# Optimization experiments

Measured on AMD Instinct MI355X. Metric: run time of the kernel, lower is better.

## Reference

```python
import jax, jax.numpy as jnp
import numpy as np

S, T, B, IN, H, O = 64, 32, 512, 66, 1024, 1024  # S == max_length


def _gru_cell(x, h, Wih, Whh, bih, bhh):
    # PyTorch GRU cell: gates ordered (r, z, n)
    gi = x @ Wih.T + bih            # [B, 3H]
    gh = h @ Whh.T + bhh            # [B, 3H]
    ir, iz, inn = jnp.split(gi, 3, axis=1)
    hr, hz, hn = jnp.split(gh, 3, axis=1)
    r = jax.nn.sigmoid(ir + hr)
    z = jax.nn.sigmoid(iz + hz)
    n = jnp.tanh(inn + r * hn)
    return (1.0 - z) * n + z * h


def setup_inputs() -> dict:
    key = jax.random.key(0)
    ks = jax.random.split(key, 20)
    s = 0.02
    return {
        "input_tensor": jax.random.normal(ks[0], (S, B, IN), jnp.float32),
        "target_tensor": jax.random.normal(ks[1], (T, B, H), jnp.float32),
        # encoder GRU
        "enc_Wih": jax.random.normal(ks[2], (3 * H, IN), jnp.float32) * s,
        "enc_Whh": jax.random.normal(ks[3], (3 * H, H), jnp.float32) * s,
        "enc_bih": jax.random.normal(ks[4], (3 * H,), jnp.float32) * s,
        "enc_bhh": jax.random.normal(ks[5], (3 * H,), jnp.float32) * s,
        # attention: Linear(2H -> max_length)
        "attn_W": jax.random.normal(ks[6], (S, 2 * H), jnp.float32) * s,
        "attn_b": jax.random.normal(ks[7], (S,), jnp.float32) * s,
        # attn_combine: Linear(2H -> H)
        "comb_W": jax.random.normal(ks[8], (H, 2 * H), jnp.float32) * s,
        "comb_b": jax.random.normal(ks[9], (H,), jnp.float32) * s,
        # decoder GRU
        "dec_Wih": jax.random.normal(ks[10], (3 * H, H), jnp.float32) * s,
        "dec_Whh": jax.random.normal(ks[11], (3 * H, H), jnp.float32) * s,
        "dec_bih": jax.random.normal(ks[12], (3 * H,), jnp.float32) * s,
        "dec_bhh": jax.random.normal(ks[13], (3 * H,), jnp.float32) * s,
        # output: Linear(H -> O)
        "out_W": jax.random.normal(ks[14], (O, H), jnp.float32) * s,
        "out_b": jax.random.normal(ks[15], (O,), jnp.float32) * s,
    }


def reference(input_tensor, target_tensor, enc_Wih, enc_Whh, enc_bih, enc_bhh,
              attn_W, attn_b, comb_W, comb_b, dec_Wih, dec_Whh, dec_bih,
              dec_bhh, out_W, out_b):
    batch = input_tensor.shape[1]
    h0 = jnp.zeros((batch, enc_Whh.shape[1]), input_tensor.dtype)

    # ---- encoder GRU over time ----
    def enc_step(h, x):
        h2 = _gru_cell(x, h, enc_Wih, enc_Whh, enc_bih, enc_bhh)
        return h2, h2

    enc_h, enc_out = jax.lax.scan(enc_step, h0, input_tensor)  # enc_out: [S, B, H]

    # ---- attention decoder, teacher forcing; loop t = 1..T-1 uses target[t-1] ----
    def dec_step(h, x):
        aw = jax.nn.softmax(jnp.concatenate([x, h], axis=1) @ attn_W.T + attn_b,
                            axis=1)                              # [B, S]
        ctx = jnp.einsum('bl,lbh->bh', aw, enc_out)              # [B, H]
        comb = jax.nn.relu(jnp.concatenate([x, ctx], axis=1) @ comb_W.T + comb_b)
        h2 = _gru_cell(comb, h, dec_Wih, dec_Whh, dec_bih, dec_bhh)
        out = jax.nn.log_softmax(h2 @ out_W.T + out_b, axis=1)   # [B, O]
        return h2, out

    _, outs = jax.lax.scan(dec_step, enc_h, target_tensor[:-1])
    # original overwrites `outputs` every step -> only last step survives
    return outs[-1]
```

## Files before the change

kernel.cpp:

```cpp
#include <hip/hip_runtime.h>
#include <hip/hip_bf16.h>
#include <math.h>

#define S_LEN 64
#define T_LEN 32
#define BATCH 512
#define IN_DIM 66
#define INP 128
#define H_DIM 1024
#define O_DIM 1024
#define H3 3072
#define NB 256
#define AUX_SC 17

typedef __attribute__((ext_vector_type(8))) short short8;
typedef __attribute__((ext_vector_type(4))) float f32x4;
typedef __attribute__((ext_vector_type(4))) unsigned short us4;

__device__ __forceinline__ unsigned short f2b(float f) {
    union { float f; unsigned u; } x; x.f = f;
    unsigned r = x.u + 0x7FFF + ((x.u >> 16) & 1);
    return (unsigned short)(r >> 16);
}
__device__ __forceinline__ float b2f(unsigned short s) {
    union { unsigned u; float f; } x; x.u = ((unsigned)s) << 16;
    return x.f;
}
template<int AUX>
__device__ __forceinline__ void gll16x(const void* g, const void* l) {
    __builtin_amdgcn_global_load_lds(
        (const __attribute__((address_space(1))) unsigned int*)g,
        (__attribute__((address_space(3))) unsigned int*)l, 16, 0, AUX);
}
__device__ __forceinline__ void gll16(const void* g, const void* l) {
    gll16x<0>(g, l);
}
__device__ __forceinline__ void store_b16_sc(unsigned short* p, unsigned v) {
    asm volatile("global_store_short %0, %1, off sc0 sc1" :: "v"(p), "v"(v) : "memory");
}

__device__ __forceinline__ void gbar_arrive(unsigned* bar) {
    __hip_atomic_fetch_add(bar, 1u, __ATOMIC_RELAXED, __HIP_MEMORY_SCOPE_AGENT);
}
__device__ __forceinline__ void gbar_wait(unsigned* bar, unsigned target) {
    while (__hip_atomic_load(bar, __ATOMIC_RELAXED, __HIP_MEMORY_SCOPE_AGENT) < target)
        __builtin_amdgcn_s_sleep(2);
}

template<int TM, int TN>
__global__ __launch_bounds__(256) void gemm_k(
    const unsigned short* __restrict__ A, int lda,
    const unsigned short* __restrict__ W, int ldw,
    const float* __restrict__ bias,
    const float* __restrict__ addf, const unsigned short* __restrict__ addb,
    int ldadd,
    float* __restrict__ Cf,
    unsigned short* __restrict__ Cb, int ldc,
    int K, int flags)
{
    constexpr int IF = TM / 16;
    constexpr int JF = TN / 64;
    constexpr int NW = TN / 4;
    constexpr int CA = TM * 4;
    constexpr int CW = TN * 4;
    __shared__ __align__(16) unsigned short As[2][TM * 32];
    __shared__ __align__(16) unsigned short Bs[2][TN * 32];

    const int bm = blockIdx.y * TM;
    const int bn = blockIdx.x * TN;
    const int t = threadIdx.x;
    const int lane = t & 63;
    const int wv = t >> 6;
    const int ln = lane & 15;
    const int quad = lane >> 4;

    f32x4 acc[IF][JF];
    #pragma unroll
    for (int i = 0; i < IF; i++)
        #pragma unroll
        for (int j = 0; j < JF; j++) {
            f32x4 z = {0.f, 0.f, 0.f, 0.f};
            acc[i][j] = z;
        }

    auto stage = [&](int buf, int k0) {
        if constexpr (CA >= 256) {
            #pragma unroll
            for (int j = 0; j < CA / 256; j++) {
                int ch = j * 256 + t;
                gll16(A + (size_t)(bm + (ch >> 2)) * lda + k0 + (ch & 3) * 8,
                      (const char*)As[buf] + (j * 4 + wv) * 1024);
            }
        } else {
            if (t < CA)
                gll16(A + (size_t)(bm + (t >> 2)) * lda + k0 + (t & 3) * 8,
                      (const char*)As[buf] + wv * 1024);
        }
        if constexpr (CW >= 256) {
            #pragma unroll
            for (int j = 0; j < CW / 256; j++) {
                int ch = j * 256 + t;
                gll16(W + (size_t)(bn + (ch >> 2)) * ldw + k0 + (ch & 3) * 8,
                      (const char*)Bs[buf] + (j * 4 + wv) * 1024);
            }
        } else {
            if (t < CW)
                gll16(W + (size_t)(bn + (t >> 2)) * ldw + k0 + (t & 3) * 8,
                      (const char*)Bs[buf] + wv * 1024);
        }
    };

    const int nt = K >> 5;
    stage(0, 0);
    __syncthreads();
    for (int i = 0; i < nt; ++i) {
        const int cur = i & 1;
        if (i + 1 < nt) stage(cur ^ 1, (i + 1) << 5);
        short8 af[IF], bf[JF];
        #pragma unroll
        for (int ii = 0; ii < IF; ii++)
            af[ii] = *(const short8*)&As[cur][(ii * 16 + ln) * 32 + quad * 8];
        #pragma unroll
        for (int j = 0; j < JF; j++)
            bf[j] = *(const short8*)&Bs[cur][(wv * NW + j * 16 + ln) * 32 + quad * 8];
        #pragma unroll
        for (int ii = 0; ii < IF; ii++)
            #pragma unroll
            for (int j = 0; j < JF; j++)
                acc[ii][j] = __builtin_amdgcn_mfma_f32_16x16x32_bf16(
                    af[ii], bf[j], acc[ii][j], 0, 0, 0);
        __syncthreads();
    }

    #pragma unroll
    for (int i = 0; i < IF; i++) {
        #pragma unroll
        for (int j = 0; j < JF; j++) {
            #pragma unroll
            for (int r = 0; r < 4; r++) {
                int m = bm + i * 16 + quad * 4 + r;
                int n = bn + wv * NW + j * 16 + ln;
                float v = acc[i][j][r];
                if (flags & 1) v += bias[n];
                if (flags & 2) v += addf[(size_t)m * ldadd + n];
                if (flags & 4) v += b2f(addb[(size_t)m * ldadd + n]);
                if (flags & 8) v = fmaxf(v, 0.f);
                if (flags & 16) Cf[(size_t)m * ldc + n] = v;
                if (flags & 32) Cb[(size_t)m * ldc + n] = f2b(v);
            }
        }
    }
}

template<int AAUX>
__device__ __forceinline__ void gru_stage(
    const unsigned short* __restrict__ A, int lda,
    const unsigned short* __restrict__ W, int ldw, int kb,
    unsigned short* As_g, unsigned short* Ws_g,
    int bm, int bn, int gt, int gwv)
{
    {
        int s = gt >> 7, r = (gt >> 2) & 31, c = gt & 3;
        gll16x<AAUX>(A + (size_t)(bm + r) * lda + kb + s * 32 + c * 8,
                     (const char*)As_g + gwv * 1024);
    }
    #pragma unroll
    for (int j = 0; j < 6; j++) {
        int ch = j * 256 + gt;
        int g2 = ch >> 9, ch2 = ch & 511;
        int s = ch2 >> 8, r = (ch2 >> 2) & 63, c = ch2 & 3;
        gll16(W + (size_t)(g2 * H_DIM + bn + r) * ldw + kb + s * 32 + c * 8,
              (const char*)Ws_g + j * 4096 + gwv * 1024);
    }
}

__device__ __forceinline__ void gru_compute(
    const unsigned short* As_g, const unsigned short* Ws_g,
    int gwv, int ln, int quad,
    f32x4 (&accR)[2], f32x4 (&accZ)[2], f32x4 (&accN)[2])
{
    #pragma unroll
    for (int sub = 0; sub < 2; sub++) {
        short8 a[2], bw[3];
        #pragma unroll
        for (int i = 0; i < 2; i++)
            a[i] = *(const short8*)&As_g[sub * 1024 + (i * 16 + ln) * 32 + quad * 8];
        #pragma unroll
        for (int g = 0; g < 3; g++)
            bw[g] = *(const short8*)&Ws_g[g * 4096 + sub * 2048 + (gwv * 16 + ln) * 32 + quad * 8];
        #pragma unroll
        for (int i = 0; i < 2; i++) {
            accR[i] = __builtin_amdgcn_mfma_f32_16x16x32_bf16(a[i], bw[0], accR[i], 0, 0, 0);
            accZ[i] = __builtin_amdgcn_mfma_f32_16x16x32_bf16(a[i], bw[1], accZ[i], 0, 0, 0);
            accN[i] = __builtin_amdgcn_mfma_f32_16x16x32_bf16(a[i], bw[2], accN[i], 0, 0, 0);
        }
    }
}

template<bool SC>
__device__ __forceinline__ void gru_finish(
    f32x4 (&accR)[2], f32x4 (&accZ)[2], f32x4 (&accN0)[2], f32x4 (&accN1)[2],
    float* red, int wg, int gwv, int lane, int ln, int quad, int bm, int bn,
    const float* __restrict__ bih, const float* __restrict__ bhh,
    const float* __restrict__ hf_in, float* __restrict__ hf_out,
    unsigned short* __restrict__ hb_out, unsigned short* __restrict__ slot)
{
    const int rb = (gwv * 64 + lane) * 33;
    if (wg == 1) {
        #pragma unroll
        for (int i = 0; i < 2; i++)
            #pragma unroll
            for (int r = 0; r < 4; r++) {
                red[rb + i * 4 + r]      = accR[i][r];
                red[rb + 8 + i * 4 + r]  = accZ[i][r];
                red[rb + 16 + i * 4 + r] = accN0[i][r];
                red[rb + 24 + i * 4 + r] = accN1[i][r];
            }
    }
    __syncthreads();
    if (wg == 0) {
        #pragma unroll
        for (int i = 0; i < 2; i++)
            #pragma unroll
            for (int r = 0; r < 4; r++) {
                accR[i][r]  += red[rb + i * 4 + r];
                accZ[i][r]  += red[rb + 8 + i * 4 + r];
                accN0[i][r] += red[rb + 16 + i * 4 + r];
                accN1[i][r] += red[rb + 24 + i * 4 + r];
            }
        const int n = bn + gwv * 16 + ln;
        const float br = bih[n] + bhh[n];
        const float bz = bih[H_DIM + n] + bhh[H_DIM + n];
        const float bi_n = bih[2 * H_DIM + n];
        const float bh_n = bhh[2 * H_DIM + n];
        #pragma unroll
        for (int i = 0; i < 2; i++) {
            #pragma unroll
            for (int r = 0; r < 4; r++) {
                const int m = bm + i * 16 + quad * 4 + r;
                const size_t idx = (size_t)m * H_DIM + n;
                float rg = 1.f / (1.f + __expf(-(accR[i][r] + br)));
                float zg = 1.f / (1.f + __expf(-(accZ[i][r] + bz)));
                float av = accN0[i][r] + bi_n + rg * (accN1[i][r] + bh_n);
                float e2 = __expf(-2.f * fabsf(av));
                float th = (1.f - e2) / (1.f + e2);
                th = av < 0.f ? -th : th;
                float o = (1.f - zg) * th + zg * hf_in[idx];
                hf_out[idx] = o;
                unsigned short ob = f2b(o);
                if (SC) store_b16_sc(hb_out + idx, (unsigned)ob);
                else    hb_out[idx] = ob;
                if (slot) slot[idx] = ob;
            }
        }
    }
}

__global__ __launch_bounds__(512) void enc_persist(
    const unsigned short* __restrict__ xbp,
    const unsigned short* __restrict__ wIhp,
    const unsigned short* __restrict__ wWhh,
    const float* __restrict__ bih, const float* __restrict__ bhh,
    float* __restrict__ h,
    unsigned short* __restrict__ hb0,
    unsigned short* __restrict__ hb1,
    unsigned short* __restrict__ encb,
    unsigned* __restrict__ bar)
{
    __shared__ __align__(16) unsigned short As2[2][2][2048];
    __shared__ __align__(16) unsigned short Ws2[2][2][12288];

    const int bid = blockIdx.x;
    const int xcd = bid & 7, sb = bid >> 3;
    const int bn = (xcd * 2 + (sb >> 4)) * 64;
    const int bm = (sb & 15) * 32;
    const int t = threadIdx.x;
    const int wg = t >> 8;
    const int gt = t & 255;
    const int lane = t & 63;
    const int gwv = gt >> 6;
    const int ln = lane & 15;
    const int quad = lane >> 4;

    unsigned short* hb[2] = {hb0, hb1};

    for (int s = 0; s < S_LEN; ++s) {
        f32x4 accR[2], accZ[2], accN0[2], accN1[2];
        #pragma unroll
        for (int i = 0; i < 2; i++) {
            f32x4 z = {0.f, 0.f, 0.f, 0.f};
            accR[i] = z; accZ[i] = z; accN0[i] = z; accN1[i] = z;
        }
        gru_stage<0>(xbp + (size_t)s * BATCH * INP, INP, wIhp, INP, wg * 64,
                     As2[wg][0], Ws2[wg][0], bm, bn, gt, gwv);
        __syncthreads();
        gru_compute(As2[wg][0], Ws2[wg][0], gwv, ln, quad, accR, accZ, accN0);
        if (t == 0 && s > 0) gbar_wait(bar, (unsigned)(s * NB));
        __syncthreads();
        const unsigned short* A1 = hb[s & 1];
        gru_stage<AUX_SC>(A1, H_DIM, wWhh, H_DIM, wg * 512,
                          As2[wg][1], Ws2[wg][1], bm, bn, gt, gwv);
        __syncthreads();
        for (int i = 0; i < 8; ++i) {
            const int cur = (i + 1) & 1;
            if (i + 1 < 8)
                gru_stage<AUX_SC>(A1, H_DIM, wWhh, H_DIM, wg * 512 + ((i + 1) << 6),
                                  As2[wg][cur ^ 1], Ws2[wg][cur ^ 1], bm, bn, gt, gwv);
            gru_compute(As2[wg][cur], Ws2[wg][cur], gwv, ln, quad, accR, accZ, accN1);
            __syncthreads();
        }
        gru_finish<true>(accR, accZ, accN0, accN1, (float*)Ws2, wg, gwv, lane,
                         ln, quad, bm, bn, bih, bhh, h, h, hb[(s + 1) & 1],
                         encb + (size_t)s * BATCH * H_DIM);
        __syncthreads();
        if (t == 0 && s < S_LEN - 1) gbar_arrive(bar);
    }
}

__global__ __launch_bounds__(512) void gru_gemm(
    const unsigned short* __restrict__ A0, int lda0,
    const unsigned short* __restrict__ W0, int ldw0, int K0,
    const unsigned short* __restrict__ A1,
    const unsigned short* __restrict__ W1,
    const float* __restrict__ bih, const float* __restrict__ bhh,
    const float* __restrict__ hf_in, float* __restrict__ hf_out,
    unsigned short* __restrict__ hb_out, unsigned short* __restrict__ slot)
{
    __shared__ __align__(16) unsigned short As2[2][2][2 * 32 * 32];
    __shared__ __align__(16) unsigned short Ws2[2][2][3 * 2 * 64 * 32];
    const int lin = blockIdx.y * gridDim.x + blockIdx.x;
    const int xcd = lin & 7, j = lin >> 3;
    const int bn = (xcd * 2 + (j & 1)) * 64;
    const int bm = (j >> 1) * 32;
    const int t = threadIdx.x;
    const int wg = t >> 8;
    const int gt = t & 255;
    const int lane = t & 63;
    const int gwv = gt >> 6;
    const int ln = lane & 15;
    const int quad = lane >> 4;

    f32x4 accR[2], accZ[2], accN0[2], accN1[2];
    #pragma unroll
    for (int i = 0; i < 2; i++) {
        f32x4 z = {0.f, 0.f, 0.f, 0.f};
        accR[i] = z; accZ[i] = z; accN0[i] = z; accN1[i] = z;
    }

    const int half0 = K0 >> 1;
    const int nt0 = half0 >> 6;
    const int nt = nt0 + 8;

    auto stg = [&](int i, int buf) {
        const unsigned short* A; int lda; const unsigned short* W; int ldw; int kb;
        if (i < nt0) { A = A0; lda = lda0; W = W0; ldw = ldw0; kb = wg * half0 + (i << 6); }
        else         { A = A1; lda = H_DIM; W = W1; ldw = H_DIM; kb = wg * 512 + ((i - nt0) << 6); }
        gru_stage<0>(A, lda, W, ldw, kb, As2[wg][buf], Ws2[wg][buf], bm, bn, gt, gwv);
    };

    stg(0, 0);
    __syncthreads();
    for (int i = 0; i < nt; ++i) {
        const int cur = i & 1;
        if (i + 1 < nt) stg(i + 1, cur ^ 1);
        if (i < nt0)
            gru_compute(As2[wg][cur], Ws2[wg][cur], gwv, ln, quad, accR, accZ, accN0);
        else
            gru_compute(As2[wg][cur], Ws2[wg][cur], gwv, ln, quad, accR, accZ, accN1);
        __syncthreads();
    }

    gru_finish<false>(accR, accZ, accN0, accN1, (float*)Ws2, wg, gwv, lane,
                      ln, quad, bm, bn, bih, bhh, hf_in, hf_out, hb_out, slot);
}

__global__ __launch_bounds__(256) void attn_ctx(
    const unsigned short* __restrict__ hb,
    const unsigned short* __restrict__ wAhT,
    const unsigned short* __restrict__ attnx_t,
    const unsigned short* __restrict__ encb,
    unsigned short* __restrict__ ctx)
{
    __shared__ float hf[H_DIM];
    __shared__ float part[4][S_LEN];
    __shared__ float awl[S_LEN];
    const int b = blockIdx.x, t = threadIdx.x;
    {
        us4 u = *(const us4*)(hb + ((size_t)b << 10) + t * 4);
        #pragma unroll
        for (int j = 0; j < 4; j++) hf[t * 4 + j] = b2f(u[j]);
    }
    __syncthreads();
    {
        const int c = t & 63, ks = (t >> 6) * 256;
        float s = 0.f;
        #pragma unroll 8
        for (int k = 0; k < 256; k++)
            s += hf[ks + k] * b2f(wAhT[(size_t)(ks + k) * S_LEN + c]);
        part[t >> 6][c] = s;
    }
    __syncthreads();
    if (t < 64) {
        float v = part[0][t] + part[1][t] + part[2][t] + part[3][t]
                + b2f(attnx_t[b * S_LEN + t]);
        float m = v;
        #pragma unroll
        for (int off = 32; off; off >>= 1) m = fmaxf(m, __shfl_xor(m, off));
        float e = __expf(v - m);
        float ss = e;
        #pragma unroll
        for (int off = 32; off; off >>= 1) ss += __shfl_xor(ss, off);
        awl[t] = e / ss;
    }
    __syncthreads();
    const int hq = t * 4;
    float s0 = 0.f, s1 = 0.f, s2 = 0.f, s3 = 0.f;
    #pragma unroll 4
    for (int l = 0; l < S_LEN; l++) {
        us4 u = *(const us4*)(encb + (((size_t)l * BATCH + b) << 10) + hq);
        float w = awl[l];
        s0 += w * b2f(u[0]); s1 += w * b2f(u[1]);
        s2 += w * b2f(u[2]); s3 += w * b2f(u[3]);
    }
    us4 o; o[0] = f2b(s0); o[1] = f2b(s1); o[2] = f2b(s2); o[3] = f2b(s3);
    *(us4*)(ctx + ((size_t)b << 10) + hq) = o;
}

__global__ __launch_bounds__(256) void cvt_all(
    const float* __restrict__ enc_Whh, const float* __restrict__ dec_Wih,
    const float* __restrict__ dec_Whh, const float* __restrict__ comb_W,
    const float* __restrict__ out_W,   const float* __restrict__ attn_W,
    const float* __restrict__ enc_Wih, const float* __restrict__ input,
    const float* __restrict__ target,
    unsigned short* __restrict__ wWhh, unsigned short* __restrict__ wDih,
    unsigned short* __restrict__ wDhh, unsigned short* __restrict__ wCc,
    unsigned short* __restrict__ wCx,  unsigned short* __restrict__ wO,
    unsigned short* __restrict__ wAx,  unsigned short* __restrict__ wAhT,
    unsigned short* __restrict__ wIhp, unsigned short* __restrict__ xbp,
    unsigned short* __restrict__ targetb)
{
    const unsigned nW = H3 * H_DIM / 4;
    const unsigned nH = H_DIM * H_DIM / 4;
    const unsigned nA = S_LEN * H_DIM / 4;
    const unsigned nI = H3 * INP / 4;
    const unsigned nX = S_LEN * BATCH * INP / 4;
    const unsigned nT = T_LEN * BATCH * H_DIM / 4;
    const unsigned total = 3 * nW + 3 * nH + 2 * nA + nI + nX + nT;

    auto plain4 = [](const float* s, unsigned short* d, unsigned i) {
        f32x4 v = *(const f32x4*)(s + (size_t)i * 4);
        us4 o;
        #pragma unroll
        for (int j = 0; j < 4; j++) o[j] = f2b(v[j]);
        *(us4*)(d + (size_t)i * 4) = o;
    };
    auto strided4 = [](const float* s, int ld, int off, int c4s,
                       unsigned short* d, unsigned i) {
        int r = i / c4s, c4 = i - r * c4s;
        f32x4 v = *(const f32x4*)(s + (size_t)r * ld + off + c4 * 4);
        us4 o;
        #pragma unroll
        for (int j = 0; j < 4; j++) o[j] = f2b(v[j]);
        *(us4*)(d + (size_t)i * 4) = o;
    };
    auto pad4 = [](const float* s, unsigned short* d, unsigned i) {
        int r = i >> 5, c = (i & 31) * 4;
        us4 o;
        #pragma unroll
        for (int j = 0; j < 4; j++) {
            int cc = c + j;
            o[j] = (cc < IN_DIM) ? f2b(s[(size_t)r * IN_DIM + cc]) : (unsigned short)0;
        }
        *(us4*)(d + (size_t)r * INP + c) = o;
    };

    for (unsigned q = blockIdx.x * blockDim.x + threadIdx.x; q < total;
         q += gridDim.x * blockDim.x) {
        unsigned i = q;
        if (i < nW) { plain4(enc_Whh, wWhh, i); continue; }  i -= nW;
        if (i < nW) { plain4(dec_Wih, wDih, i); continue; }  i -= nW;
        if (i < nW) { plain4(dec_Whh, wDhh, i); continue; }  i -= nW;
        if (i < nH) { strided4(comb_W, 2 * H_DIM, H_DIM, H_DIM / 4, wCc, i); continue; }  i -= nH;
        if (i < nH) { strided4(comb_W, 2 * H_DIM, 0, H_DIM / 4, wCx, i); continue; }  i -= nH;
        if (i < nH) { plain4(out_W, wO, i); continue; }  i -= nH;
        if (i < nA) { strided4(attn_W, 2 * H_DIM, 0, H_DIM / 4, wAx, i); continue; }  i -= nA;
        if (i < nA) {
            int idx = i * 4, k = idx >> 6, c = idx & 63;
            us4 o;
            #pragma unroll
            for (int j = 0; j < 4; j++)
                o[j] = f2b(attn_W[(size_t)(c + j) * 2 * H_DIM + H_DIM + k]);
            *(us4*)(wAhT + idx) = o;
            continue;
        }  i -= nA;
        if (i < nI) { pad4(enc_Wih, wIhp, i); continue; }  i -= nI;
        if (i < nX) { pad4(input, xbp, i); continue; }  i -= nX;
        plain4(target, targetb, i);
    }
}

__global__ void log_softmax1024(float* __restrict__ x)
{
    __shared__ float red[256];
    float* xr = x + (size_t)blockIdx.x * O_DIM;
    int t = threadIdx.x;
    float m = -1e30f;
    for (int i = t; i < O_DIM; i += 256) m = fmaxf(m, xr[i]);
    red[t] = m; __syncthreads();
    for (int s2 = 128; s2 > 0; s2 >>= 1) {
        if (t < s2) red[t] = fmaxf(red[t], red[t + s2]);
        __syncthreads();
    }
    m = red[0];
    __syncthreads();
    float s = 0.f;
    for (int i = t; i < O_DIM; i += 256) s += expf(xr[i] - m);
    red[t] = s; __syncthreads();
    for (int s2 = 128; s2 > 0; s2 >>= 1) {
        if (t < s2) red[t] += red[t + s2];
        __syncthreads();
    }
    float lse = m + logf(red[0]);
    __syncthreads();
    for (int i = t; i < O_DIM; i += 256) xr[i] = xr[i] - lse;
}

extern "C" void kernel_launch(void* const* d_in, const int* in_sizes, int n_in,
                              void* d_out, int out_size, void* d_ws, size_t ws_size,
                              hipStream_t stream)
{
    const float* input   = (const float*)d_in[0];
    const float* target  = (const float*)d_in[1];
    const float* enc_Wih = (const float*)d_in[2];
    const float* enc_Whh = (const float*)d_in[3];
    const float* enc_bih = (const float*)d_in[4];
    const float* enc_bhh = (const float*)d_in[5];
    const float* attn_W  = (const float*)d_in[6];
    const float* attn_b  = (const float*)d_in[7];
    const float* comb_W  = (const float*)d_in[8];
    const float* comb_b  = (const float*)d_in[9];
    const float* dec_Wih = (const float*)d_in[10];
    const float* dec_Whh = (const float*)d_in[11];
    const float* dec_bih = (const float*)d_in[12];
    const float* dec_bhh = (const float*)d_in[13];
    const float* out_W   = (const float*)d_in[14];
    const float* out_b   = (const float*)d_in[15];
    float* out = (float*)d_out;

    char* p = (char*)d_ws;
    auto alloc = [&](size_t bytes) {
        char* r = p; p += (bytes + 255) & ~(size_t)255; return r;
    };
    unsigned short* wWhh  = (unsigned short*)alloc((size_t)H3 * H_DIM * 2);
    unsigned short* wDih  = (unsigned short*)alloc((size_t)H3 * H_DIM * 2);
    unsigned short* wDhh  = (unsigned short*)alloc((size_t)H3 * H_DIM * 2);
    unsigned short* wCc   = (unsigned short*)alloc((size_t)H_DIM * H_DIM * 2);
    unsigned short* wCx   = (unsigned short*)alloc((size_t)H_DIM * H_DIM * 2);
    unsigned short* wO    = (unsigned short*)alloc((size_t)O_DIM * H_DIM * 2);
    unsigned short* wAhT  = (unsigned short*)alloc((size_t)H_DIM * S_LEN * 2);
    unsigned short* wAx   = (unsigned short*)alloc((size_t)S_LEN * H_DIM * 2);
    unsigned short* wIhp  = (unsigned short*)alloc((size_t)H3 * INP * 2);
    unsigned short* xbp   = (unsigned short*)alloc((size_t)S_LEN * BATCH * INP * 2);
    unsigned short* encb  = (unsigned short*)alloc((size_t)S_LEN * BATCH * H_DIM * 2);
    unsigned short* combx = (unsigned short*)alloc((size_t)(T_LEN - 1) * BATCH * H_DIM * 2);
    unsigned short* attnx = (unsigned short*)alloc((size_t)(T_LEN - 1) * BATCH * S_LEN * 2);
    float*          h     = (float*)alloc((size_t)BATCH * H_DIM * 4);
    unsigned short* hbA   = (unsigned short*)alloc((size_t)BATCH * H_DIM * 2);
    unsigned short* hbB   = (unsigned short*)alloc((size_t)BATCH * H_DIM * 2);
    unsigned short* ctx   = (unsigned short*)alloc((size_t)BATCH * H_DIM * 2);
    unsigned short* comb  = (unsigned short*)alloc((size_t)BATCH * H_DIM * 2);
    unsigned*       bar   = (unsigned*)alloc(512);
    unsigned short* targetb = encb;

    const dim3 blk(256);

    hipMemsetAsync(h,   0, (size_t)BATCH * H_DIM * 4, stream);
    hipMemsetAsync(hbA, 0, (size_t)BATCH * H_DIM * 2, stream);
    hipMemsetAsync(bar, 0, 512, stream);

    cvt_all<<<2048, blk, 0, stream>>>(
        enc_Whh, dec_Wih, dec_Whh, comb_W, out_W, attn_W, enc_Wih, input, target,
        wWhh, wDih, wDhh, wCc, wCx, wO, wAx, wAhT, wIhp, xbp, targetb);

    const int MT = (T_LEN - 1) * BATCH;
    gemm_k<64, 64><<<dim3(1, MT / 64), blk, 0, stream>>>(
        targetb, H_DIM, wAx, H_DIM, attn_b,
        nullptr, nullptr, 0, nullptr, attnx, S_LEN, H_DIM, 1 | 32);
    gemm_k<128, 128><<<dim3(H_DIM / 128, MT / 128), blk, 0, stream>>>(
        targetb, H_DIM, wCx, H_DIM, comb_b,
        nullptr, nullptr, 0, nullptr, combx, H_DIM, H_DIM, 1 | 32);

    enc_persist<<<NB, 512, 0, stream>>>(
        xbp, wIhp, wWhh, enc_bih, enc_bhh, h, hbA, hbB, encb, bar);

    const dim3 grid_gru(H_DIM / 64, BATCH / 32);
    const dim3 blk512(512);
    unsigned short* hcur = hbA;
    unsigned short* hnxt = hbB;
    for (int t = 0; t < T_LEN - 1; t++) {
        attn_ctx<<<BATCH, blk, 0, stream>>>(
            hcur, wAhT, attnx + (size_t)t * BATCH * S_LEN, encb, ctx);
        gemm_k<32, 64><<<dim3(H_DIM / 64, BATCH / 32), blk, 0, stream>>>(
            ctx, H_DIM, wCc, H_DIM, nullptr,
            nullptr, combx + (size_t)t * BATCH * H_DIM, H_DIM,
            nullptr, comb, H_DIM, H_DIM, 4 | 8 | 32);
        gru_gemm<<<grid_gru, blk512, 0, stream>>>(
            comb, H_DIM, wDih, H_DIM, H_DIM,
            hcur, wDhh, dec_bih, dec_bhh, h, h, hnxt, nullptr);
        unsigned short* tmp = hcur; hcur = hnxt; hnxt = tmp;
    }

    gemm_k<32, 64><<<dim3(O_DIM / 64, BATCH / 32), blk, 0, stream>>>(
        hcur, H_DIM, wO, H_DIM, out_b,
        nullptr, nullptr, 0, out, nullptr, O_DIM, H_DIM, 1 | 16);
    log_softmax1024<<<BATCH, blk, 0, stream>>>(out);
}
```

Before: 3.104 ms.

## Replace persistent encoder kernel with per-step GRU launches and smaller tiles

Removes the persistent encoder kernel, which used a global atomic barrier and coherent stores. Each encoder timestep now launches the generic gru_gemm. gru_gemm changes to 32x32 output tiles with 256 threads and drops the XCD-aware block remapping. This avoids spin-wait barrier cost and cache-bypass stores, at the price of 64 extra kernel launches and smaller tiles that reuse weights less.

```diff
diff --git a/kernel.cpp b/kernel.cpp
--- a/kernel.cpp
+++ b/kernel.cpp
@@ -10,8 +10,6 @@
 #define H_DIM 1024
 #define O_DIM 1024
 #define H3 3072
-#define NB 256
-#define AUX_SC 17
 
 typedef __attribute__((ext_vector_type(8))) short short8;
 typedef __attribute__((ext_vector_type(4))) float f32x4;
@@ -26,25 +24,10 @@
     union { unsigned u; float f; } x; x.u = ((unsigned)s) << 16;
     return x.f;
 }
-template<int AUX>
-__device__ __forceinline__ void gll16x(const void* g, const void* l) {
+__device__ __forceinline__ void gll16(const void* g, const void* l) {
     __builtin_amdgcn_global_load_lds(
         (const __attribute__((address_space(1))) unsigned int*)g,
-        (__attribute__((address_space(3))) unsigned int*)l, 16, 0, AUX);
-}
-__device__ __forceinline__ void gll16(const void* g, const void* l) {
-    gll16x<0>(g, l);
-}
-__device__ __forceinline__ void store_b16_sc(unsigned short* p, unsigned v) {
-    asm volatile("global_store_short %0, %1, off sc0 sc1" :: "v"(p), "v"(v) : "memory");
-}
-
-__device__ __forceinline__ void gbar_arrive(unsigned* bar) {
-    __hip_atomic_fetch_add(bar, 1u, __ATOMIC_RELAXED, __HIP_MEMORY_SCOPE_AGENT);
-}
-__device__ __forceinline__ void gbar_wait(unsigned* bar, unsigned target) {
-    while (__hip_atomic_load(bar, __ATOMIC_RELAXED, __HIP_MEMORY_SCOPE_AGENT) < target)
-        __builtin_amdgcn_s_sleep(2);
+        (__attribute__((address_space(3))) unsigned int*)l, 16, 0, 0);
 }
 
 template<int TM, int TN>
@@ -152,25 +135,27 @@
     }
 }
 
-template<int AAUX>
 __device__ __forceinline__ void gru_stage(
     const unsigned short* __restrict__ A, int lda,
     const unsigned short* __restrict__ W, int ldw, int kb,
     unsigned short* As_g, unsigned short* Ws_g,
-    int bm, int bn, int gt, int gwv)
-{
-    {
-        int s = gt >> 7, r = (gt >> 2) & 31, c = gt & 3;
-        gll16x<AAUX>(A + (size_t)(bm + r) * lda + kb + s * 32 + c * 8,
-                     (const char*)As_g + gwv * 1024);
+    int bm, int bn, int gt)
+{
+    const int gwv = gt >> 6;
+    #pragma unroll
+    for (int j = 0; j < 2; j++) {
+        int ch = j * 128 + gt;
+        int s = ch >> 7, r = (ch >> 2) & 31, c = ch & 3;
+        gll16(A + (size_t)(bm + r) * lda + kb + s * 32 + c * 8,
+              (const char*)As_g + j * 2048 + gwv * 1024);
     }
     #pragma unroll
     for (int j = 0; j < 6; j++) {
-        int ch = j * 256 + gt;
-        int g2 = ch >> 9, ch2 = ch & 511;
-        int s = ch2 >> 8, r = (ch2 >> 2) & 63, c = ch2 & 3;
-        gll16(W + (size_t)(g2 * H_DIM + bn + r) * ldw + kb + s * 32 + c * 8,
-              (const char*)Ws_g + j * 4096 + gwv * 1024);
+        int ch = j * 128 + gt;
+        int g = ch >> 8, ch2 = ch & 255;
+        int s = ch2 >> 7, w = (ch2 >> 2) & 31, c = ch2 & 3;
+        gll16(W + (size_t)(g * H_DIM + bn + w) * ldw + kb + s * 32 + c * 8,
+              (const char*)Ws_g + j * 2048 + gwv * 1024);
     }
 }
 
@@ -187,7 +172,7 @@
             a[i] = *(const short8*)&As_g[sub * 1024 + (i * 16 + ln) * 32 + quad * 8];
         #pragma unroll
         for (int g = 0; g < 3; g++)
-            bw[g] = *(const short8*)&Ws_g[g * 4096 + sub * 2048 + (gwv * 16 + ln) * 32 + quad * 8];
+            bw[g] = *(const short8*)&Ws_g[g * 2048 + sub * 1024 + (gwv * 16 + ln) * 32 + quad * 8];
         #pragma unroll
         for (int i = 0; i < 2; i++) {
             accR[i] = __builtin_amdgcn_mfma_f32_16x16x32_bf16(a[i], bw[0], accR[i], 0, 0, 0);
@@ -197,14 +182,58 @@
     }
 }
 
-template<bool SC>
-__device__ __forceinline__ void gru_finish(
-    f32x4 (&accR)[2], f32x4 (&accZ)[2], f32x4 (&accN0)[2], f32x4 (&accN1)[2],
-    float* red, int wg, int gwv, int lane, int ln, int quad, int bm, int bn,
+__global__ __launch_bounds__(256) void gru_gemm(
+    const unsigned short* __restrict__ A0, int lda0,
+    const unsigned short* __restrict__ W0, int ldw0, int K0,
+    const unsigned short* __restrict__ A1,
+    const unsigned short* __restrict__ W1,
     const float* __restrict__ bih, const float* __restrict__ bhh,
     const float* __restrict__ hf_in, float* __restrict__ hf_out,
     unsigned short* __restrict__ hb_out, unsigned short* __restrict__ slot)
 {
+    __shared__ __align__(16) unsigned short As2[2][2][2048];
+    __shared__ __align__(16) unsigned short Ws2[2][2][6144];
+    const int bn = blockIdx.x * 32;
+    const int bm = blockIdx.y * 32;
+    const int t = threadIdx.x;
+    const int wg = t >> 7;
+    const int gt = t & 127;
+    const int lane = t & 63;
+    const int gwv = gt >> 6;
+    const int ln = lane & 15;
+    const int quad = lane >> 4;
+
+    f32x4 accR[2], accZ[2], accN0[2], accN1[2];
+    #pragma unroll
+    for (int i = 0; i < 2; i++) {
+        f32x4 z = {0.f, 0.f, 0.f, 0.f};
+        accR[i] = z; accZ[i] = z; accN0[i] = z; accN1[i] = z;
+    }
+
+    const int half0 = K0 >> 1;
+    const int nt0 = half0 >> 6;
+    const int nt = nt0 + 8;
+
+    auto stg = [&](int i, int buf) {
+        const unsigned short* A; int lda; const unsigned short* W; int ldw; int kb;
+        if (i < nt0) { A = A0; lda = lda0; W = W0; ldw = ldw0; kb = wg * half0 + (i << 6); }
+        else         { A = A1; lda = H_DIM; W = W1; ldw = H_DIM; kb = wg * 512 + ((i - nt0) << 6); }
+        gru_stage(A, lda, W, ldw, kb, As2[wg][buf], Ws2[wg][buf], bm, bn, gt);
+    };
+
+    stg(0, 0);
+    __syncthreads();
+    for (int i = 0; i < nt; ++i) {
+        const int cur = i & 1;
+        if (i + 1 < nt) stg(i + 1, cur ^ 1);
+        if (i < nt0)
+            gru_compute(As2[wg][cur], Ws2[wg][cur], gwv, ln, quad, accR, accZ, accN0);
+        else
+            gru_compute(As2[wg][cur], Ws2[wg][cur], gwv, ln, quad, accR, accZ, accN1);
+        __syncthreads();
+    }
+
+    float* red = (float*)Ws2;
     const int rb = (gwv * 64 + lane) * 33;
     if (wg == 1) {
         #pragma unroll
@@ -248,130 +277,11 @@
                 float o = (1.f - zg) * th + zg * hf_in[idx];
                 hf_out[idx] = o;
                 unsigned short ob = f2b(o);
-                if (SC) store_b16_sc(hb_out + idx, (unsigned)ob);
-                else    hb_out[idx] = ob;
+                hb_out[idx] = ob;
                 if (slot) slot[idx] = ob;
             }
         }
     }
-}
-
-__global__ __launch_bounds__(512) void enc_persist(
-    const unsigned short* __restrict__ xbp,
-    const unsigned short* __restrict__ wIhp,
-    const unsigned short* __restrict__ wWhh,
-    const float* __restrict__ bih, const float* __restrict__ bhh,
-    float* __restrict__ h,
-    unsigned short* __restrict__ hb0,
-    unsigned short* __restrict__ hb1,
-    unsigned short* __restrict__ encb,
-    unsigned* __restrict__ bar)
-{
-    __shared__ __align__(16) unsigned short As2[2][2][2048];
-    __shared__ __align__(16) unsigned short Ws2[2][2][12288];
-
-    const int bid = blockIdx.x;
-    const int xcd = bid & 7, sb = bid >> 3;
-    const int bn = (xcd * 2 + (sb >> 4)) * 64;
-    const int bm = (sb & 15) * 32;
-    const int t = threadIdx.x;
-    const int wg = t >> 8;
-    const int gt = t & 255;
-    const int lane = t & 63;
-    const int gwv = gt >> 6;
-    const int ln = lane & 15;
-    const int quad = lane >> 4;
-
-    unsigned short* hb[2] = {hb0, hb1};
-
-    for (int s = 0; s < S_LEN; ++s) {
-        f32x4 accR[2], accZ[2], accN0[2], accN1[2];
-        #pragma unroll
-        for (int i = 0; i < 2; i++) {
-            f32x4 z = {0.f, 0.f, 0.f, 0.f};
-            accR[i] = z; accZ[i] = z; accN0[i] = z; accN1[i] = z;
-        }
-        gru_stage<0>(xbp + (size_t)s * BATCH * INP, INP, wIhp, INP, wg * 64,
-                     As2[wg][0], Ws2[wg][0], bm, bn, gt, gwv);
-        __syncthreads();
-        gru_compute(As2[wg][0], Ws2[wg][0], gwv, ln, quad, accR, accZ, accN0);
-        if (t == 0 && s > 0) gbar_wait(bar, (unsigned)(s * NB));
-        __syncthreads();
-        const unsigned short* A1 = hb[s & 1];
-        gru_stage<AUX_SC>(A1, H_DIM, wWhh, H_DIM, wg * 512,
-                          As2[wg][1], Ws2[wg][1], bm, bn, gt, gwv);
-        __syncthreads();
-        for (int i = 0; i < 8; ++i) {
-            const int cur = (i + 1) & 1;
-            if (i + 1 < 8)
-                gru_stage<AUX_SC>(A1, H_DIM, wWhh, H_DIM, wg * 512 + ((i + 1) << 6),
-                                  As2[wg][cur ^ 1], Ws2[wg][cur ^ 1], bm, bn, gt, gwv);
-            gru_compute(As2[wg][cur], Ws2[wg][cur], gwv, ln, quad, accR, accZ, accN1);
-            __syncthreads();
-        }
-        gru_finish<true>(accR, accZ, accN0, accN1, (float*)Ws2, wg, gwv, lane,
-                         ln, quad, bm, bn, bih, bhh, h, h, hb[(s + 1) & 1],
-                         encb + (size_t)s * BATCH * H_DIM);
-        __syncthreads();
-        if (t == 0 && s < S_LEN - 1) gbar_arrive(bar);
-    }
-}
-
-__global__ __launch_bounds__(512) void gru_gemm(
-    const unsigned short* __restrict__ A0, int lda0,
-    const unsigned short* __restrict__ W0, int ldw0, int K0,
-    const unsigned short* __restrict__ A1,
-    const unsigned short* __restrict__ W1,
-    const float* __restrict__ bih, const float* __restrict__ bhh,
-    const float* __restrict__ hf_in, float* __restrict__ hf_out,
-    unsigned short* __restrict__ hb_out, unsigned short* __restrict__ slot)
-{
-    __shared__ __align__(16) unsigned short As2[2][2][2 * 32 * 32];
-    __shared__ __align__(16) unsigned short Ws2[2][2][3 * 2 * 64 * 32];
-    const int lin = blockIdx.y * gridDim.x + blockIdx.x;
-    const int xcd = lin & 7, j = lin >> 3;
-    const int bn = (xcd * 2 + (j & 1)) * 64;
-    const int bm = (j >> 1) * 32;
-    const int t = threadIdx.x;
-    const int wg = t >> 8;
-    const int gt = t & 255;
-    const int lane = t & 63;
-    const int gwv = gt >> 6;
-    const int ln = lane & 15;
-    const int quad = lane >> 4;
-
-    f32x4 accR[2], accZ[2], accN0[2], accN1[2];
-    #pragma unroll
-    for (int i = 0; i < 2; i++) {
-        f32x4 z = {0.f, 0.f, 0.f, 0.f};
-        accR[i] = z; accZ[i] = z; accN0[i] = z; accN1[i] = z;
-    }
-
-    const int half0 = K0 >> 1;
-    const int nt0 = half0 >> 6;
-    const int nt = nt0 + 8;
-
-    auto stg = [&](int i, int buf) {
-        const unsigned short* A; int lda; const unsigned short* W; int ldw; int kb;
-        if (i < nt0) { A = A0; lda = lda0; W = W0; ldw = ldw0; kb = wg * half0 + (i << 6); }
-        else         { A = A1; lda = H_DIM; W = W1; ldw = H_DIM; kb = wg * 512 + ((i - nt0) << 6); }
-        gru_stage<0>(A, lda, W, ldw, kb, As2[wg][buf], Ws2[wg][buf], bm, bn, gt, gwv);
-    };
-
-    stg(0, 0);
-    __syncthreads();
-    for (int i = 0; i < nt; ++i) {
-        const int cur = i & 1;
-        if (i + 1 < nt) stg(i + 1, cur ^ 1);
-        if (i < nt0)
-            gru_compute(As2[wg][cur], Ws2[wg][cur], gwv, ln, quad, accR, accZ, accN0);
-        else
-            gru_compute(As2[wg][cur], Ws2[wg][cur], gwv, ln, quad, accR, accZ, accN1);
-        __syncthreads();
-    }
-
-    gru_finish<false>(accR, accZ, accN0, accN1, (float*)Ws2, wg, gwv, lane,
-                      ln, quad, bm, bn, bih, bhh, hf_in, hf_out, hb_out, slot);
 }
 
 __global__ __launch_bounds__(256) void attn_ctx(
@@ -569,14 +479,12 @@
     unsigned short* hbB   = (unsigned short*)alloc((size_t)BATCH * H_DIM * 2);
     unsigned short* ctx   = (unsigned short*)alloc((size_t)BATCH * H_DIM * 2);
     unsigned short* comb  = (unsigned short*)alloc((size_t)BATCH * H_DIM * 2);
-    unsigned*       bar   = (unsigned*)alloc(512);
     unsigned short* targetb = encb;
 
     const dim3 blk(256);
 
     hipMemsetAsync(h,   0, (size_t)BATCH * H_DIM * 4, stream);
     hipMemsetAsync(hbA, 0, (size_t)BATCH * H_DIM * 2, stream);
-    hipMemsetAsync(bar, 0, 512, stream);
 
     cvt_all<<<2048, blk, 0, stream>>>(
         enc_Whh, dec_Wih, dec_Whh, comb_W, out_W, attn_W, enc_Wih, input, target,
@@ -590,13 +498,18 @@
         targetb, H_DIM, wCx, H_DIM, comb_b,
         nullptr, nullptr, 0, nullptr, combx, H_DIM, H_DIM, 1 | 32);
 
-    enc_persist<<<NB, 512, 0, stream>>>(
-        xbp, wIhp, wWhh, enc_bih, enc_bhh, h, hbA, hbB, encb, bar);
-
-    const dim3 grid_gru(H_DIM / 64, BATCH / 32);
-    const dim3 blk512(512);
+    const dim3 grid_gru(H_DIM / 32, BATCH / 32);
     unsigned short* hcur = hbA;
     unsigned short* hnxt = hbB;
+
+    for (int s = 0; s < S_LEN; s++) {
+        gru_gemm<<<grid_gru, blk, 0, stream>>>(
+            xbp + (size_t)s * BATCH * INP, INP, wIhp, INP, INP,
+            hcur, wWhh, enc_bih, enc_bhh, h, h, hnxt,
+            encb + (size_t)s * BATCH * H_DIM);
+        unsigned short* tmp = hcur; hcur = hnxt; hnxt = tmp;
+    }
+
     for (int t = 0; t < T_LEN - 1; t++) {
         attn_ctx<<<BATCH, blk, 0, stream>>>(
             hcur, wAhT, attnx + (size_t)t * BATCH * S_LEN, encb, ctx);
@@ -604,7 +517,7 @@
             ctx, H_DIM, wCc, H_DIM, nullptr,
             nullptr, combx + (size_t)t * BATCH * H_DIM, H_DIM,
             nullptr, comb, H_DIM, H_DIM, 4 | 8 | 32);
-        gru_gemm<<<grid_gru, blk512, 0, stream>>>(
+        gru_gemm<<<grid_gru, blk, 0, stream>>>(
             comb, H_DIM, wDih, H_DIM, H_DIM,
             hcur, wDhh, dec_bih, dec_bhh, h, h, hnxt, nullptr);
         unsigned short* tmp = hcur; hcur = hnxt; hnxt = tmp;
```

After: 3.002 ms. 3.3% less time.
